# Performance work log

Measured on AMD Instinct MI355X. Metric: run time of the kernel, lower is better.

The kernel has to match this reference:

```python
import jax, jax.numpy as jnp
import numpy as np

SEQ_LEN = 8192
HEAD_DIM = 128


def setup_inputs() -> dict:
    key = jax.random.key(0)
    kq, kk, kv = jax.random.split(key, 3)
    q = jax.random.normal(kq, (SEQ_LEN, HEAD_DIM), dtype=jnp.float32)
    k = jax.random.normal(kk, (SEQ_LEN, HEAD_DIM), dtype=jnp.float32)
    v = jax.random.normal(kv, (SEQ_LEN, HEAD_DIM), dtype=jnp.float32)
    return {"q": q, "k": k, "v": v}


def reference(q, k, v):
    # FlashAttention computes exact softmax attention; the blocked loops with
    # online max/sum rescaling in the source are an exact reformulation of:
    #   O = softmax(Q K^T) V
    # NOTE: the original module applies no 1/sqrt(d) scaling, so neither do we.
    s = jnp.einsum('nd,md->nm', q, k)          # [N, N] scores
    p = jax.nn.softmax(s, axis=-1)             # stable softmax (online in src)
    return jnp.einsum('nm,md->nd', p, v)       # [N, d]
```

## Files before the change

### kernel.cpp

```cpp
#include <hip/hip_runtime.h>

#define N_SEQ 8192
#define HDIM  128

typedef _Float16 half8v  __attribute__((ext_vector_type(8)));
typedef float    floatx16 __attribute__((ext_vector_type(16)));
typedef unsigned int uint32;

__global__ void prep_kv(const float* __restrict__ K, const float* __restrict__ V,
                        _Float16* __restrict__ K16s, _Float16* __restrict__ Vs) {
    __shared__ float Kl[32 * 132];
    __shared__ float Vl[32 * 132];
    const int t  = threadIdx.x;
    const int nt = blockIdx.x;
    const int n0 = nt * 32;
    #pragma unroll
    for (int kk = 0; kk < 4; kk++) {
        int idx = t + 256 * kk;
        int nl = idx >> 5, c4 = idx & 31;
        float4 f = *(((const float4*)(K + (size_t)(n0 + nl) * HDIM)) + c4);
        float* dk = &Kl[nl * 132 + c4 * 4];
        dk[0] = f.x; dk[1] = f.y; dk[2] = f.z; dk[3] = f.w;
        float4 g = *(((const float4*)(V + (size_t)(n0 + nl) * HDIM)) + c4);
        float* dv = &Vl[nl * 132 + c4 * 4];
        dv[0] = g.x; dv[1] = g.y; dv[2] = g.z; dv[3] = g.w;
    }
    __syncthreads();
    #pragma unroll
    for (int rep = 0; rep < 2; rep++) {
        int ch = t + rep * 256;
        int kc = ch >> 6, lane = ch & 63, l31 = lane & 31, q5 = (lane >> 5) & 1;
        half8v h;
        #pragma unroll
        for (int j = 0; j < 8; j++) h[j] = (_Float16)Kl[l31 * 132 + kc * 16 + q5 * 8 + j];
        *(half8v*)(K16s + (((size_t)nt * 8 + kc) * 64 + lane) * 8) = h;
    }
    #pragma unroll
    for (int rep = 0; rep < 2; rep++) {
        int ch = t + rep * 256;
        int dt = ch >> 7, kc2 = (ch >> 6) & 1, lane = ch & 63, l31 = lane & 31, q5 = (lane >> 5) & 1;
        half8v h;
        #pragma unroll
        for (int j = 0; j < 8; j++) h[j] = (_Float16)Vl[(kc2 * 16 + q5 * 8 + j) * 132 + dt * 32 + l31];
        *(half8v*)(Vs + ((((size_t)nt * 4 + dt) * 2 + kc2) * 64 + lane) * 8) = h;
    }
}

static __device__ __forceinline__ void stage_tile(
        const _Float16* __restrict__ K16s, const _Float16* __restrict__ Vs,
        _Float16* lds, size_t nt, int wv, int lane) {
    #pragma unroll
    for (int i = 0; i < 4; i++) {
        const int c = wv * 4 + i;
        const _Float16* base = (c < 8) ? (K16s + (nt * 8 + c) * 512)
                                       : (Vs + (nt * 8 + (size_t)(c - 8)) * 512);
        __builtin_amdgcn_global_load_lds(
            (const __attribute__((address_space(1))) void*)(base + lane * 8),
            (__attribute__((address_space(3))) void*)(lds + c * 512),
            16, 0, 0);
    }
}

static __device__ __forceinline__ void do_pv(const half8v (&vsrc)[8], const uint32 (&hpk)[8],
                                             floatx16 (&oacc)[4], int q5) {
    #pragma unroll
    for (int kc2 = 0; kc2 < 2; kc2++) {
        uint32 pass0 = q5 ? hpk[4 * kc2 + 0] : hpk[4 * kc2 + 2];
        uint32 pass1 = q5 ? hpk[4 * kc2 + 1] : hpk[4 * kc2 + 3];
        uint32 r0 = (uint32)__shfl_xor((int)pass0, 32, 64);
        uint32 r1 = (uint32)__shfl_xor((int)pass1, 32, 64);
        uint32 b0 = q5 ? r0 : hpk[4 * kc2 + 0];
        uint32 b1 = q5 ? r1 : hpk[4 * kc2 + 1];
        uint32 b2 = q5 ? hpk[4 * kc2 + 2] : r0;
        uint32 b3 = q5 ? hpk[4 * kc2 + 3] : r1;
        uint4 bu = make_uint4(b0, b1, b2, b3);
        half8v bfrag = __builtin_bit_cast(half8v, bu);
        #pragma unroll
        for (int dt = 0; dt < 4; dt++)
            oacc[dt] = __builtin_amdgcn_mfma_f32_32x32x16_f16(vsrc[dt * 2 + kc2], bfrag, oacc[dt], 0, 0, 0);
    }
}

template <bool DO_PV>
static __device__ __forceinline__ void pipe_step(
        const half8v (&qf)[8], half8v (&vin)[8], const half8v (&vprev)[8],
        floatx16 (&oacc)[4], uint32 (&hpk)[8],
        float& runm, float& lsum, float& palpha, bool& pflag,
        const _Float16* lds, int lane, int q5) {
    half8v kf[8];
    #pragma unroll
    for (int kc = 0; kc < 8; kc++)
        kf[kc] = *(const half8v*)(lds + kc * 512 + lane * 8);
    #pragma unroll
    for (int j = 0; j < 8; j++)
        vin[j] = *(const half8v*)(lds + (8 + j) * 512 + lane * 8);
    if (pflag) {
        #pragma unroll
        for (int dt = 0; dt < 4; dt++)
            #pragma unroll
            for (int r = 0; r < 16; r++) oacc[dt][r] *= palpha;
        pflag = false;
    }
    if (DO_PV) do_pv(vprev, hpk, oacc, q5);
    floatx16 s0, s1;
    #pragma unroll
    for (int r = 0; r < 16; r++) { s0[r] = 0.0f; s1[r] = 0.0f; }
    #pragma unroll
    for (int kc = 0; kc < 4; kc++)
        s0 = __builtin_amdgcn_mfma_f32_32x32x16_f16(kf[kc], qf[kc], s0, 0, 0, 0);
    #pragma unroll
    for (int kc = 4; kc < 8; kc++)
        s1 = __builtin_amdgcn_mfma_f32_32x32x16_f16(kf[kc], qf[kc], s1, 0, 0, 0);
    float sc[16];
    #pragma unroll
    for (int r = 0; r < 16; r++) sc[r] = s0[r] + s1[r];
    float tm[8];
    #pragma unroll
    for (int r = 0; r < 8; r++) tm[r] = fmaxf(sc[r], sc[r + 8]);
    #pragma unroll
    for (int w = 4; w; w >>= 1)
        #pragma unroll
        for (int r = 0; r < w; r++) tm[r] = fmaxf(tm[r], tm[r + w]);
    float cmax = fmaxf(tm[0], __shfl_xor(tm[0], 32, 64));
    if (__any(cmax > runm + 12.0f)) {
        const float mnew = fmaxf(runm, cmax);
        palpha = __builtin_amdgcn_exp2f(runm - mnew);
        runm = mnew;
        lsum *= palpha;
        pflag = true;
    }
    float p[16];
    #pragma unroll
    for (int r = 0; r < 16; r++) p[r] = __builtin_amdgcn_exp2f(sc[r] - runm);
    float ts[8];
    #pragma unroll
    for (int r = 0; r < 8; r++) ts[r] = p[r] + p[r + 8];
    #pragma unroll
    for (int w = 4; w; w >>= 1)
        #pragma unroll
        for (int r = 0; r < w; r++) ts[r] += ts[r + w];
    lsum += ts[0];
    #pragma unroll
    for (int t2 = 0; t2 < 8; t2++) {
        auto pk = __builtin_amdgcn_cvt_pkrtz(p[2 * t2], p[2 * t2 + 1]);
        hpk[t2] = __builtin_bit_cast(uint32, pk);
    }
}

__launch_bounds__(256, 2)
__global__ void fa_main(const float* __restrict__ Qp, const _Float16* __restrict__ K16s,
                        const _Float16* __restrict__ Vs, float* __restrict__ Opart,
                        float* __restrict__ lpart, float* __restrict__ mpart, int tiles) {
    __shared__ _Float16 ldsbuf[2][8192];
    const int tid  = threadIdx.x;
    const int lane = tid & 63;
    const int wv   = tid >> 6;
    const int l31  = lane & 31;
    const int q5   = lane >> 5;
    const int sp   = blockIdx.x;
    const int m0   = blockIdx.y * 128 + wv * 32;
    const float LOG2E = 1.44269504088896f;

    half8v qf[8];
    {
        const float* qrow = Qp + (size_t)(m0 + l31) * HDIM;
        #pragma unroll
        for (int kc = 0; kc < 8; kc++) {
            const float4 a = *(const float4*)(qrow + kc * 16 + q5 * 8);
            const float4 b = *(const float4*)(qrow + kc * 16 + q5 * 8 + 4);
            half8v h;
            h[0] = (_Float16)(a.x * LOG2E); h[1] = (_Float16)(a.y * LOG2E);
            h[2] = (_Float16)(a.z * LOG2E); h[3] = (_Float16)(a.w * LOG2E);
            h[4] = (_Float16)(b.x * LOG2E); h[5] = (_Float16)(b.y * LOG2E);
            h[6] = (_Float16)(b.z * LOG2E); h[7] = (_Float16)(b.w * LOG2E);
            qf[kc] = h;
        }
    }

    floatx16 oacc[4];
    #pragma unroll
    for (int dt = 0; dt < 4; dt++)
        #pragma unroll
        for (int r = 0; r < 16; r++) oacc[dt][r] = 0.0f;

    float runm = -3.0e38f;
    float lsum = 0.0f;
    float palpha = 0.0f;
    bool  pflag = false;
    uint32 hpk[8];
    half8v va[8], vb[8];

    const size_t nt0 = (size_t)sp * tiles;

    stage_tile(K16s, Vs, ldsbuf[0], nt0, wv, lane);
    __syncthreads();
    stage_tile(K16s, Vs, ldsbuf[1], nt0 + 1, wv, lane);
    pipe_step<false>(qf, va, va, oacc, hpk, runm, lsum, palpha, pflag, ldsbuf[0], lane, q5);
    __syncthreads();
    for (int p = 0; p < (tiles - 2) / 2; p++) {
        stage_tile(K16s, Vs, ldsbuf[0], nt0 + 2 + 2 * p, wv, lane);
        pipe_step<true>(qf, vb, va, oacc, hpk, runm, lsum, palpha, pflag, ldsbuf[1], lane, q5);
        __syncthreads();
        stage_tile(K16s, Vs, ldsbuf[1], nt0 + 3 + 2 * p, wv, lane);
        pipe_step<true>(qf, va, vb, oacc, hpk, runm, lsum, palpha, pflag, ldsbuf[0], lane, q5);
        __syncthreads();
    }
    pipe_step<true>(qf, vb, va, oacc, hpk, runm, lsum, palpha, pflag, ldsbuf[1], lane, q5);
    if (pflag) {
        #pragma unroll
        for (int dt = 0; dt < 4; dt++)
            #pragma unroll
            for (int r = 0; r < 16; r++) oacc[dt][r] *= palpha;
    }
    do_pv(vb, hpk, oacc, q5);

    float ltot = lsum + __shfl_xor(lsum, 32, 64);
    if (lane < 32) {
        lpart[(size_t)sp * N_SEQ + m0 + l31] = ltot;
        mpart[(size_t)sp * N_SEQ + m0 + l31] = runm;
    }
    #pragma unroll
    for (int dt = 0; dt < 4; dt++)
        #pragma unroll
        for (int r = 0; r < 16; r++) {
            int d = dt * 32 + (r & 3) + 8 * (r >> 2) + 4 * q5;
            Opart[((size_t)sp * HDIM + d) * N_SEQ + m0 + l31] = oacc[dt][r];
        }
}

template <int S>
__global__ void fa_merge(const float* __restrict__ Opart, const float* __restrict__ lpart,
                         const float* __restrict__ mpart, float* __restrict__ Out) {
    __shared__ float lds[64 * 33];
    const int t  = threadIdx.x;
    const int m0 = blockIdx.x * 64;
    const int i  = t & 63;
    const int g  = t >> 6;
    const int m  = m0 + i;
    const int d0 = blockIdx.y * 32 + g * 8;

    float mv[S], lv[S];
    #pragma unroll
    for (int s = 0; s < S; s++) {
        mv[s] = mpart[(size_t)s * N_SEQ + m];
        lv[s] = lpart[(size_t)s * N_SEQ + m];
    }
    float M = -3.0e38f;
    #pragma unroll
    for (int s = 0; s < S; s++) M = fmaxf(M, mv[s]);
    float wsc[S];
    float L = 0.0f;
    #pragma unroll
    for (int s = 0; s < S; s++) {
        wsc[s] = __builtin_amdgcn_exp2f(mv[s] - M);
        L += lv[s] * wsc[s];
    }
    const float inv = 1.0f / L;

    float acc[8];
    #pragma unroll
    for (int dd = 0; dd < 8; dd++) acc[dd] = 0.0f;
    #pragma unroll
    for (int s = 0; s < S; s++) {
        const float ww = wsc[s] * inv;
        #pragma unroll
        for (int dd = 0; dd < 8; dd++)
            acc[dd] += Opart[((size_t)s * HDIM + d0 + dd) * N_SEQ + m] * ww;
    }
    #pragma unroll
    for (int dd = 0; dd < 8; dd++) lds[i * 33 + g * 8 + dd] = acc[dd];
    __syncthreads();
    const int mi = t >> 2, c = t & 3;
    float4 v0, v1;
    const float* row = &lds[mi * 33 + c * 8];
    v0.x = row[0]; v0.y = row[1]; v0.z = row[2]; v0.w = row[3];
    v1.x = row[4]; v1.y = row[5]; v1.z = row[6]; v1.w = row[7];
    float* outp = Out + (size_t)(m0 + mi) * HDIM + blockIdx.y * 32 + c * 8;
    *(float4*)(outp)     = v0;
    *(float4*)(outp + 4) = v1;
}

__global__ void fa_naive(const float* __restrict__ Q, const float* __restrict__ K,
                         const float* __restrict__ V, float* __restrict__ O) {
    const int m = blockIdx.x;
    const int t = threadIdx.x;
    __shared__ float qs[HDIM];
    __shared__ float ps[256];
    __shared__ float red[256];
    if (t < HDIM) qs[t] = Q[(size_t)m * HDIM + t] * 1.44269504f;
    __syncthreads();
    float om = -3.0e38f, ls = 0.0f, oa = 0.0f;
    for (int nb = 0; nb < N_SEQ; nb += 256) {
        const float* kr = K + (size_t)(nb + t) * HDIM;
        float s = 0.0f;
        #pragma unroll 8
        for (int d = 0; d < HDIM; d++) s += qs[d] * kr[d];
        red[t] = s; __syncthreads();
        for (int st = 128; st > 0; st >>= 1) { if (t < st) red[t] = fmaxf(red[t], red[t + st]); __syncthreads(); }
        float cm = red[0];
        __syncthreads();
        float mn = fmaxf(om, cm);
        float al = __builtin_amdgcn_exp2f(om - mn);
        om = mn;
        float pp = __builtin_amdgcn_exp2f(s - mn);
        ps[t] = pp; red[t] = pp; __syncthreads();
        for (int st = 128; st > 0; st >>= 1) { if (t < st) red[t] += red[t + st]; __syncthreads(); }
        float csum = red[0];
        ls = ls * al + csum;
        if (t < HDIM) {
            float acc = 0.0f;
            for (int j = 0; j < 256; j++) acc += ps[j] * V[(size_t)(nb + j) * HDIM + t];
            oa = oa * al + acc;
        }
        __syncthreads();
    }
    if (t < HDIM) O[(size_t)m * HDIM + t] = oa / ls;
}

extern "C" void kernel_launch(void* const* d_in, const int* in_sizes, int n_in,
                              void* d_out, int out_size, void* d_ws, size_t ws_size,
                              hipStream_t stream) {
    const float* q = (const float*)d_in[0];
    const float* k = (const float*)d_in[1];
    const float* v = (const float*)d_in[2];
    float* out = (float*)d_out;

    const size_t MB = 1024ull * 1024ull;
    int S = 0;
    for (int s = 8; s >= 1; s >>= 1) {
        size_t need = 4 * MB + (size_t)s * (4 * MB + 64 * 1024);
        if (ws_size >= need) { S = s; break; }
    }
    if (S == 0) {
        fa_naive<<<N_SEQ, 256, 0, stream>>>(q, k, v, out);
        return;
    }
    char* ws = (char*)d_ws;
    _Float16* K16s = (_Float16*)ws;
    _Float16* Vs   = (_Float16*)(ws + 2 * MB);
    float* Opart   = (float*)(ws + 4 * MB);
    float* lpart   = (float*)(ws + 4 * MB + (size_t)S * 4 * MB);
    float* mpart   = lpart + (size_t)S * N_SEQ;

    prep_kv<<<dim3(N_SEQ / 32), dim3(256), 0, stream>>>(k, v, K16s, Vs);
    fa_main<<<dim3(S, N_SEQ / 128), dim3(256), 0, stream>>>(q, K16s, Vs, Opart, lpart, mpart, (N_SEQ / 32) / S);
    dim3 mg(N_SEQ / 64, HDIM / 32);
    switch (S) {
        case 8:  fa_merge<8> <<<mg, dim3(256), 0, stream>>>(Opart, lpart, mpart, out); break;
        case 4:  fa_merge<4> <<<mg, dim3(256), 0, stream>>>(Opart, lpart, mpart, out); break;
        case 2:  fa_merge<2> <<<mg, dim3(256), 0, stream>>>(Opart, lpart, mpart, out); break;
        default: fa_merge<1> <<<mg, dim3(256), 0, stream>>>(Opart, lpart, mpart, out); break;
    }
}
```

Measured before the change: 120.2 us.

## Store partial outputs row-major via LDS transpose and vectorize merge

The main kernel now stages each wave's accumulator tile through LDS, one quarter at a time, and writes partial outputs in row-major [split][row][dim] order with float4 stores, replacing scattered column-major scalar stores. The merge kernel then reads contiguous float4 rows per split and writes output directly, without an LDS transpose, using a 1D grid of 32 rows per block. This is meant to make global stores and loads coalesced on both sides. The cost is extra LDS traffic and barriers in the epilogue of the main kernel, and it relies on ldsbuf being large enough for 32x132 floats.

```diff
diff --git a/kernel.cpp b/kernel.cpp
--- a/kernel.cpp
+++ b/kernel.cpp
@@ -219,25 +219,41 @@
         lpart[(size_t)sp * N_SEQ + m0 + l31] = ltot;
         mpart[(size_t)sp * N_SEQ + m0 + l31] = runm;
     }
-    #pragma unroll
-    for (int dt = 0; dt < 4; dt++)
-        #pragma unroll
-        for (int r = 0; r < 16; r++) {
-            int d = dt * 32 + (r & 3) + 8 * (r >> 2) + 4 * q5;
-            Opart[((size_t)sp * HDIM + d) * N_SEQ + m0 + l31] = oacc[dt][r];
-        }
+
+    float* ldsf = (float*)ldsbuf;
+    const size_t obase = ((size_t)sp * N_SEQ + blockIdx.y * 128) * HDIM;
+    #pragma unroll
+    for (int qtr = 0; qtr < 4; qtr++) {
+        __syncthreads();
+        if (wv == qtr) {
+            #pragma unroll
+            for (int dt = 0; dt < 4; dt++)
+                #pragma unroll
+                for (int g = 0; g < 4; g++) {
+                    float4 v = make_float4(oacc[dt][4 * g + 0], oacc[dt][4 * g + 1],
+                                           oacc[dt][4 * g + 2], oacc[dt][4 * g + 3]);
+                    *(float4*)&ldsf[l31 * 132 + dt * 32 + g * 8 + q5 * 4] = v;
+                }
+        }
+        __syncthreads();
+        const int lrow = wv * 8 + (lane >> 3);
+        const int c    = lane & 7;
+        #pragma unroll
+        for (int j = 0; j < 4; j++) {
+            float4 v = *(const float4*)&ldsf[lrow * 132 + (j * 8 + c) * 4];
+            *(float4*)&Opart[obase + (size_t)(qtr * 32 + lrow) * HDIM + (j * 8 + c) * 4] = v;
+        }
+    }
 }
 
 template <int S>
-__global__ void fa_merge(const float* __restrict__ Opart, const float* __restrict__ lpart,
-                         const float* __restrict__ mpart, float* __restrict__ Out) {
-    __shared__ float lds[64 * 33];
-    const int t  = threadIdx.x;
-    const int m0 = blockIdx.x * 64;
-    const int i  = t & 63;
-    const int g  = t >> 6;
-    const int m  = m0 + i;
-    const int d0 = blockIdx.y * 32 + g * 8;
+__global__ __launch_bounds__(256) void fa_merge(const float* __restrict__ Opart,
+                                                const float* __restrict__ lpart,
+                                                const float* __restrict__ mpart,
+                                                float* __restrict__ Out) {
+    const int t = threadIdx.x;
+    const int m = blockIdx.x * 32 + (t >> 3);
+    const int c = t & 7;
 
     float mv[S], lv[S];
     #pragma unroll
@@ -257,27 +273,24 @@
     }
     const float inv = 1.0f / L;
 
-    float acc[8];
-    #pragma unroll
-    for (int dd = 0; dd < 8; dd++) acc[dd] = 0.0f;
+    float4 acc[4];
+    #pragma unroll
+    for (int j = 0; j < 4; j++) acc[j] = make_float4(0.f, 0.f, 0.f, 0.f);
     #pragma unroll
     for (int s = 0; s < S; s++) {
         const float ww = wsc[s] * inv;
-        #pragma unroll
-        for (int dd = 0; dd < 8; dd++)
-            acc[dd] += Opart[((size_t)s * HDIM + d0 + dd) * N_SEQ + m] * ww;
-    }
-    #pragma unroll
-    for (int dd = 0; dd < 8; dd++) lds[i * 33 + g * 8 + dd] = acc[dd];
-    __syncthreads();
-    const int mi = t >> 2, c = t & 3;
-    float4 v0, v1;
-    const float* row = &lds[mi * 33 + c * 8];
-    v0.x = row[0]; v0.y = row[1]; v0.z = row[2]; v0.w = row[3];
-    v1.x = row[4]; v1.y = row[5]; v1.z = row[6]; v1.w = row[7];
-    float* outp = Out + (size_t)(m0 + mi) * HDIM + blockIdx.y * 32 + c * 8;
-    *(float4*)(outp)     = v0;
-    *(float4*)(outp + 4) = v1;
+        const float* src = Opart + ((size_t)s * N_SEQ + m) * HDIM;
+        #pragma unroll
+        for (int j = 0; j < 4; j++) {
+            float4 v = *(const float4*)&src[(j * 8 + c) * 4];
+            acc[j].x += v.x * ww; acc[j].y += v.y * ww;
+            acc[j].z += v.z * ww; acc[j].w += v.w * ww;
+        }
+    }
+    float* dst = Out + (size_t)m * HDIM;
+    #pragma unroll
+    for (int j = 0; j < 4; j++)
+        *(float4*)&dst[(j * 8 + c) * 4] = acc[j];
 }
 
 __global__ void fa_naive(const float* __restrict__ Q, const float* __restrict__ K,
@@ -344,7 +357,7 @@
 
     prep_kv<<<dim3(N_SEQ / 32), dim3(256), 0, stream>>>(k, v, K16s, Vs);
     fa_main<<<dim3(S, N_SEQ / 128), dim3(256), 0, stream>>>(q, K16s, Vs, Opart, lpart, mpart, (N_SEQ / 32) / S);
-    dim3 mg(N_SEQ / 64, HDIM / 32);
+    dim3 mg(N_SEQ / 32);
     switch (S) {
         case 8:  fa_merge<8> <<<mg, dim3(256), 0, stream>>>(Opart, lpart, mpart, out); break;
         case 4:  fa_merge<4> <<<mg, dim3(256), 0, stream>>>(Opart, lpart, mpart, out); break;
```

After: 120.8 us. About the same (+0.5%).
